# Kernel optimization log

Hardware: AMD Instinct MI355X
Metric: run time of the kernel (lower is better)

## Reference

```python
import jax, jax.numpy as jnp
import numpy as np
from jax import lax

H = 0.00048828125  # grid spacing h = 1/2048 (init kwarg)
B, G = 16, 2050    # batch, padded grid size; interior = G-2 = 2048


def _stencil(u, f_int, h2):
    # 4-neighbor Jacobi update on padded field u [B,1,G,G] -> [B,1,G-2,G-2]
    nbr = (u[..., :-2, 1:-1] + u[..., 2:, 1:-1] +
           u[..., 1:-1, :-2] + u[..., 1:-1, 2:])
    return (nbr + h2 * f_int) * 0.25


def setup_inputs() -> dict:
    key = jax.random.key(0)
    k1, k2 = jax.random.split(key)
    pre = jax.random.normal(k1, (B, 1, G, G), dtype=jnp.float32)
    f = jax.random.normal(k2, (B, 1, G, G), dtype=jnp.float32)
    return {"pre": pre, "f": f, "max_iter": 50}


def reference(pre, f, max_iter):
    h2 = jnp.asarray(H * H, dtype=pre.dtype)
    f_int = f[..., 1:-1, 1:-1]  # fixed interior source term

    w = _stencil(pre, f_int, h2)  # first step uses pre directly

    def body(w, _):
        # hard_encode: zero-pad border (gd = 0.0 default), then stencil step
        u = jnp.pad(w, ((0, 0), (0, 0), (1, 1), (1, 1)))
        return _stencil(u, f_int, h2), None

    w, _ = lax.scan(body, w, None, length=max_iter - 1)
    return w
```

## Files before the change

### kernel.cpp

```cpp
#include <hip/hip_runtime.h>


#define NDIM 2048
#define GDIM 2050
#define BATCH 16
#define H2 2.384185791015625e-07f

#define BSTRIDE 84
#define NSLOT 42

__device__ __forceinline__ float f4get(float4 v, int k) {
    return k == 0 ? v.x : k == 1 ? v.y : k == 2 ? v.z : v.w;
}

template<bool FIRST, bool EDGE>
__device__ __forceinline__ void run_block(const float* __restrict__ src,
                                          const float* __restrict__ fg,
                                          float* __restrict__ out, int iters,
                                          float* __restrict__ buf,
                                          float4* __restrict__ colL,
                                          float4* __restrict__ colR)
{
    const int tid = threadIdx.x;
    const int R0 = blockIdx.y * 64, C0 = blockIdx.x * 64;
    const int b = blockIdx.z;
    const float* sb = src + (size_t)b * (FIRST ? (size_t)GDIM * GDIM
                                               : (size_t)NDIM * NDIM);
    const float* fb = fg + (size_t)b * GDIM * GDIM;

    const bool active = tid < 400;
    const int cy = tid / 20, cx = tid - cy * 20;
    const int gy0 = R0 - 8 + 4 * cy, gx0 = C0 - 8 + 4 * cx;

    float cur[16], fv[16];
    unsigned mwb = 0;

    if (active) {
        if (!FIRST && !EDGE) {
            #pragma unroll
            for (int i = 0; i < 4; ++i) {
                float4 t = *(const float4*)&sb[(size_t)(gy0 + i) * NDIM + gx0];
                cur[i*4+0] = t.x; cur[i*4+1] = t.y;
                cur[i*4+2] = t.z; cur[i*4+3] = t.w;
            }
        } else {
            #pragma unroll
            for (int i = 0; i < 4; ++i) {
                #pragma unroll
                for (int j = 0; j < 4; ++j) {
                    int gy = gy0 + i, gx = gx0 + j;
                    float v = 0.0f;
                    if (FIRST) {
                        if (!EDGE || ((unsigned)(gy + 1) < (unsigned)GDIM &&
                                      (unsigned)(gx + 1) < (unsigned)GDIM))
                            v = sb[(size_t)(gy + 1) * GDIM + (gx + 1)];
                    } else {
                        if ((unsigned)gy < (unsigned)NDIM &&
                            (unsigned)gx < (unsigned)NDIM)
                            v = sb[(size_t)gy * NDIM + gx];
                    }
                    cur[i*4+j] = v;
                }
            }
        }
        #pragma unroll
        for (int i = 0; i < 4; ++i) {
            #pragma unroll
            for (int j = 0; j < 4; ++j) {
                int gy = gy0 + i, gx = gx0 + j;
                float vf = 0.0f;
                if (!EDGE) {
                    vf = fb[(size_t)(gy + 1) * GDIM + (gx + 1)];
                } else {
                    bool ok = (unsigned)gy < (unsigned)NDIM &&
                              (unsigned)gx < (unsigned)NDIM;
                    if (ok) vf = fb[(size_t)(gy + 1) * GDIM + (gx + 1)];
                    mwb |= (ok ? 1u : 0u) << (i*4+j);
                }
                fv[i*4+j] = vf;
            }
        }
        *(float4*)&buf[(2*cy+1)*BSTRIDE + 4*cx] =
            make_float4(cur[0], cur[1], cur[2], cur[3]);
        *(float4*)&buf[(2*cy+2)*BSTRIDE + 4*cx] =
            make_float4(cur[12], cur[13], cur[14], cur[15]);
        colL[cy*21+cx]     = make_float4(cur[0], cur[4], cur[8],  cur[12]);
        colR[cy*21+cx+1]   = make_float4(cur[3], cur[7], cur[11], cur[15]);
    } else if (tid < 480) {
        int role = (tid - 400) / 20;
        int k = tid - 400 - role * 20;
        float v[4];
        if (role < 2) {
            int gy = (role == 0) ? R0 - 9 : R0 + 72;
            int gxb = C0 - 8 + 4 * k;
            if (!FIRST && !EDGE) {
                float4 t = *(const float4*)&sb[(size_t)gy * NDIM + gxb];
                v[0] = t.x; v[1] = t.y; v[2] = t.z; v[3] = t.w;
            } else {
                #pragma unroll
                for (int j = 0; j < 4; ++j) {
                    int gx = gxb + j; float vv = 0.0f;
                    if (FIRST) {
                        if (!EDGE || ((unsigned)(gy + 1) < (unsigned)GDIM &&
                                      (unsigned)(gx + 1) < (unsigned)GDIM))
                            vv = sb[(size_t)(gy + 1) * GDIM + (gx + 1)];
                    } else {
                        if ((unsigned)gy < (unsigned)NDIM &&
                            (unsigned)gx < (unsigned)NDIM)
                            vv = sb[(size_t)gy * NDIM + gx];
                    }
                    v[j] = vv;
                }
            }
            int slot = (role == 0) ? 0 : (NSLOT - 1);
            *(float4*)&buf[slot * BSTRIDE + 4 * k] =
                make_float4(v[0], v[1], v[2], v[3]);
        } else {
            int gx = (role == 2) ? C0 - 9 : C0 + 72;
            int gyb = R0 - 8 + 4 * k;
            #pragma unroll
            for (int i = 0; i < 4; ++i) {
                int gy = gyb + i; float vv = 0.0f;
                if (FIRST) {
                    if (!EDGE || ((unsigned)(gy + 1) < (unsigned)GDIM &&
                                  (unsigned)(gx + 1) < (unsigned)GDIM))
                        vv = sb[(size_t)(gy + 1) * GDIM + (gx + 1)];
                } else {
                    if ((unsigned)gy < (unsigned)NDIM &&
                        (unsigned)gx < (unsigned)NDIM)
                        vv = sb[(size_t)gy * NDIM + gx];
                }
                v[i] = vv;
            }
            if (role == 2) colR[k*21 + 0]  = make_float4(v[0], v[1], v[2], v[3]);
            else           colL[k*21 + 20] = make_float4(v[0], v[1], v[2], v[3]);
        }
    }
    __syncthreads();

    for (int s = 0; s < iters; ++s) {
        float4 Nv, Sv, Wv, Ev;
        if (active) {
            Nv = *(const float4*)&buf[(2*cy)   * BSTRIDE + 4*cx];
            Sv = *(const float4*)&buf[(2*cy+3) * BSTRIDE + 4*cx];
            Wv = colR[cy*21+cx];
            Ev = colL[cy*21+cx+1];
        }
        __syncthreads();
        if (active) {
            float pn[4] = { Nv.x, Nv.y, Nv.z, Nv.w };
            #pragma unroll
            for (int i = 0; i < 4; ++i) {
                float t[4];
                #pragma unroll
                for (int j = 0; j < 4; ++j) {
                    float nn = pn[j];
                    float sv = (i == 3) ? f4get(Sv, j) : cur[(i+1)*4+j];
                    float wv = (j == 0) ? f4get(Wv, i) : cur[i*4+j-1];
                    float ev = (j == 3) ? f4get(Ev, i) : cur[i*4+j+1];
                    float val = (nn + sv + wv + ev + H2 * fv[i*4+j]) * 0.25f;
                    if (EDGE) val = ((mwb >> (i*4+j)) & 1u) ? val : 0.0f;
                    t[j] = val;
                }
                #pragma unroll
                for (int j = 0; j < 4; ++j) {
                    pn[j] = cur[i*4+j];
                    cur[i*4+j] = t[j];
                }
            }
            *(float4*)&buf[(2*cy+1)*BSTRIDE + 4*cx] =
                make_float4(cur[0], cur[1], cur[2], cur[3]);
            *(float4*)&buf[(2*cy+2)*BSTRIDE + 4*cx] =
                make_float4(cur[12], cur[13], cur[14], cur[15]);
            colL[cy*21+cx]   = make_float4(cur[0], cur[4], cur[8],  cur[12]);
            colR[cy*21+cx+1] = make_float4(cur[3], cur[7], cur[11], cur[15]);
        }
        __syncthreads();
    }

    if (active && cy >= 2 && cy < 18 && cx >= 2 && cx < 18) {
        float* ob = out + (size_t)b * NDIM * NDIM;
        const int oy0 = R0 + 4 * (cy - 2);
        const int ox0 = C0 + 4 * (cx - 2);
        #pragma unroll
        for (int i = 0; i < 4; ++i)
            *(float4*)&ob[(size_t)(oy0 + i) * NDIM + ox0] =
                make_float4(cur[i*4+0], cur[i*4+1], cur[i*4+2], cur[i*4+3]);
    }
}

template<bool FIRST>
__global__ __launch_bounds__(512)
void jacobi_fused(const float* __restrict__ src, const float* __restrict__ f,
                  float* __restrict__ out, int iters)
{
    __shared__ __align__(16) float buf[NSLOT * BSTRIDE];
    __shared__ float4 colL[20 * 21];
    __shared__ float4 colR[20 * 21];
    const bool edge = (blockIdx.x == 0) || (blockIdx.x == 31) ||
                      (blockIdx.y == 0) || (blockIdx.y == 31);
    if (edge) run_block<FIRST, true >(src, f, out, iters, buf, colL, colR);
    else      run_block<FIRST, false>(src, f, out, iters, buf, colL, colR);
}

extern "C" void kernel_launch(void* const* d_in, const int* in_sizes, int n_in,
                              void* d_out, int out_size, void* d_ws, size_t ws_size,
                              hipStream_t stream) {
    const float* pre = (const float*)d_in[0];
    const float* f   = (const float*)d_in[1];
    float* out = (float*)d_out;
    float* ws  = (float*)d_ws;

    dim3 block(512, 1, 1);
    dim3 grid(32, 32, BATCH);

    hipLaunchKernelGGL(jacobi_fused<true>,  grid, block, 0, stream, pre, f, ws,  9);
    hipLaunchKernelGGL(jacobi_fused<false>, grid, block, 0, stream, ws,  f, out, 9);
    hipLaunchKernelGGL(jacobi_fused<false>, grid, block, 0, stream, out, f, ws,  9);
    hipLaunchKernelGGL(jacobi_fused<false>, grid, block, 0, stream, ws,  f, out, 9);
    hipLaunchKernelGGL(jacobi_fused<false>, grid, block, 0, stream, out, f, ws,  9);
    hipLaunchKernelGGL(jacobi_fused<false>, grid, block, 0, stream, ws,  f, out, 5);
}
```

Measured before the change: 2.673 ms.

## Use 4x8 per-thread register tiles with 256-thread blocks in fused Jacobi

Each thread now holds an 8-row by 4-column tile in registers instead of 4x4, so a 256-thread block covers the same 80x80 halo tile with 200 compute threads. This halves the number of shared-memory halo exchanges per point and the number of participating threads per barrier, and it uses a launch bound of 256 threads with 4 blocks per CU. The shared-memory strides change and the row-halo loads lose their float4 fast path, since helper threads now loop over the 80 halo tasks. More registers per thread (32 cur plus 32 fv) could limit occupancy or cause spills.

Result: slower. 3.865 ms (+44.6%).

```diff
diff --git a/kernel.cpp b/kernel.cpp
--- a/kernel.cpp
+++ b/kernel.cpp
@@ -6,8 +6,9 @@
 #define BATCH 16
 #define H2 2.384185791015625e-07f
 
-#define BSTRIDE 84
-#define NSLOT 42
+#define BSTRIDE 88
+#define NSLOT 22
+#define CSTRIDE 28
 
 __device__ __forceinline__ float f4get(float4 v, int k) {
     return k == 0 ? v.x : k == 1 ? v.y : k == 2 ? v.z : v.w;
@@ -28,24 +29,24 @@
                                                : (size_t)NDIM * NDIM);
     const float* fb = fg + (size_t)b * GDIM * GDIM;
 
-    const bool active = tid < 400;
-    const int cy = tid / 20, cx = tid - cy * 20;
-    const int gy0 = R0 - 8 + 4 * cy, gx0 = C0 - 8 + 4 * cx;
-
-    float cur[16], fv[16];
+    const bool active = tid < 200;
+    const int chy = tid / 20, chx = tid - chy * 20;
+    const int gy0 = R0 - 8 + 8 * chy, gx0 = C0 - 8 + 4 * chx;
+
+    float cur[32], fv[32];
     unsigned mwb = 0;
 
     if (active) {
         if (!FIRST && !EDGE) {
             #pragma unroll
-            for (int i = 0; i < 4; ++i) {
+            for (int i = 0; i < 8; ++i) {
                 float4 t = *(const float4*)&sb[(size_t)(gy0 + i) * NDIM + gx0];
                 cur[i*4+0] = t.x; cur[i*4+1] = t.y;
                 cur[i*4+2] = t.z; cur[i*4+3] = t.w;
             }
         } else {
             #pragma unroll
-            for (int i = 0; i < 4; ++i) {
+            for (int i = 0; i < 8; ++i) {
                 #pragma unroll
                 for (int j = 0; j < 4; ++j) {
                     int gy = gy0 + i, gx = gx0 + j;
@@ -64,7 +65,7 @@
             }
         }
         #pragma unroll
-        for (int i = 0; i < 4; ++i) {
+        for (int i = 0; i < 8; ++i) {
             #pragma unroll
             for (int j = 0; j < 4; ++j) {
                 int gy = gy0 + i, gx = gx0 + j;
@@ -80,23 +81,22 @@
                 fv[i*4+j] = vf;
             }
         }
-        *(float4*)&buf[(2*cy+1)*BSTRIDE + 4*cx] =
+        *(float4*)&buf[(2*chy+1)*BSTRIDE + 4*chx] =
             make_float4(cur[0], cur[1], cur[2], cur[3]);
-        *(float4*)&buf[(2*cy+2)*BSTRIDE + 4*cx] =
-            make_float4(cur[12], cur[13], cur[14], cur[15]);
-        colL[cy*21+cx]     = make_float4(cur[0], cur[4], cur[8],  cur[12]);
-        colR[cy*21+cx+1]   = make_float4(cur[3], cur[7], cur[11], cur[15]);
-    } else if (tid < 480) {
-        int role = (tid - 400) / 20;
-        int k = tid - 400 - role * 20;
-        float v[4];
-        if (role < 2) {
-            int gy = (role == 0) ? R0 - 9 : R0 + 72;
-            int gxb = C0 - 8 + 4 * k;
-            if (!FIRST && !EDGE) {
-                float4 t = *(const float4*)&sb[(size_t)gy * NDIM + gxb];
-                v[0] = t.x; v[1] = t.y; v[2] = t.z; v[3] = t.w;
-            } else {
+        *(float4*)&buf[(2*chy+2)*BSTRIDE + 4*chx] =
+            make_float4(cur[28], cur[29], cur[30], cur[31]);
+        colL[(2*chy+0)*CSTRIDE + chx]   = make_float4(cur[0],  cur[4],  cur[8],  cur[12]);
+        colL[(2*chy+1)*CSTRIDE + chx]   = make_float4(cur[16], cur[20], cur[24], cur[28]);
+        colR[(2*chy+0)*CSTRIDE + chx+1] = make_float4(cur[3],  cur[7],  cur[11], cur[15]);
+        colR[(2*chy+1)*CSTRIDE + chx+1] = make_float4(cur[19], cur[23], cur[27], cur[31]);
+    } else {
+        for (int task = tid - 200; task < 80; task += 56) {
+            int kind = task / 20;
+            int k = task - kind * 20;
+            float v[4];
+            if (kind < 2) {
+                int gy = (kind == 0) ? R0 - 9 : R0 + 72;
+                int gxb = C0 - 8 + 4 * k;
                 #pragma unroll
                 for (int j = 0; j < 4; ++j) {
                     int gx = gxb + j; float vv = 0.0f;
@@ -111,53 +111,57 @@
                     }
                     v[j] = vv;
                 }
-            }
-            int slot = (role == 0) ? 0 : (NSLOT - 1);
-            *(float4*)&buf[slot * BSTRIDE + 4 * k] =
-                make_float4(v[0], v[1], v[2], v[3]);
-        } else {
-            int gx = (role == 2) ? C0 - 9 : C0 + 72;
-            int gyb = R0 - 8 + 4 * k;
-            #pragma unroll
-            for (int i = 0; i < 4; ++i) {
-                int gy = gyb + i; float vv = 0.0f;
-                if (FIRST) {
-                    if (!EDGE || ((unsigned)(gy + 1) < (unsigned)GDIM &&
-                                  (unsigned)(gx + 1) < (unsigned)GDIM))
-                        vv = sb[(size_t)(gy + 1) * GDIM + (gx + 1)];
-                } else {
-                    if ((unsigned)gy < (unsigned)NDIM &&
-                        (unsigned)gx < (unsigned)NDIM)
-                        vv = sb[(size_t)gy * NDIM + gx];
-                }
-                v[i] = vv;
-            }
-            if (role == 2) colR[k*21 + 0]  = make_float4(v[0], v[1], v[2], v[3]);
-            else           colL[k*21 + 20] = make_float4(v[0], v[1], v[2], v[3]);
+                int slot = (kind == 0) ? 0 : (NSLOT - 1);
+                *(float4*)&buf[slot * BSTRIDE + 4 * k] =
+                    make_float4(v[0], v[1], v[2], v[3]);
+            } else {
+                int gx = (kind == 2) ? C0 - 9 : C0 + 72;
+                int gyb = R0 - 8 + 4 * k;
+                #pragma unroll
+                for (int i = 0; i < 4; ++i) {
+                    int gy = gyb + i; float vv = 0.0f;
+                    if (FIRST) {
+                        if (!EDGE || ((unsigned)(gy + 1) < (unsigned)GDIM &&
+                                      (unsigned)(gx + 1) < (unsigned)GDIM))
+                            vv = sb[(size_t)(gy + 1) * GDIM + (gx + 1)];
+                    } else {
+                        if ((unsigned)gy < (unsigned)NDIM &&
+                            (unsigned)gx < (unsigned)NDIM)
+                            vv = sb[(size_t)gy * NDIM + gx];
+                    }
+                    v[i] = vv;
+                }
+                if (kind == 2) colR[k * CSTRIDE + 0]  = make_float4(v[0], v[1], v[2], v[3]);
+                else           colL[k * CSTRIDE + 20] = make_float4(v[0], v[1], v[2], v[3]);
+            }
         }
     }
     __syncthreads();
 
     for (int s = 0; s < iters; ++s) {
-        float4 Nv, Sv, Wv, Ev;
+        float4 Nv, Sv, Wv0, Wv1, Ev0, Ev1;
         if (active) {
-            Nv = *(const float4*)&buf[(2*cy)   * BSTRIDE + 4*cx];
-            Sv = *(const float4*)&buf[(2*cy+3) * BSTRIDE + 4*cx];
-            Wv = colR[cy*21+cx];
-            Ev = colL[cy*21+cx+1];
+            Nv  = *(const float4*)&buf[(2*chy)   * BSTRIDE + 4*chx];
+            Sv  = *(const float4*)&buf[(2*chy+3) * BSTRIDE + 4*chx];
+            Wv0 = colR[(2*chy+0)*CSTRIDE + chx];
+            Wv1 = colR[(2*chy+1)*CSTRIDE + chx];
+            Ev0 = colL[(2*chy+0)*CSTRIDE + chx+1];
+            Ev1 = colL[(2*chy+1)*CSTRIDE + chx+1];
         }
         __syncthreads();
         if (active) {
             float pn[4] = { Nv.x, Nv.y, Nv.z, Nv.w };
             #pragma unroll
-            for (int i = 0; i < 4; ++i) {
+            for (int i = 0; i < 8; ++i) {
                 float t[4];
                 #pragma unroll
                 for (int j = 0; j < 4; ++j) {
                     float nn = pn[j];
-                    float sv = (i == 3) ? f4get(Sv, j) : cur[(i+1)*4+j];
-                    float wv = (j == 0) ? f4get(Wv, i) : cur[i*4+j-1];
-                    float ev = (j == 3) ? f4get(Ev, i) : cur[i*4+j+1];
+                    float sv = (i == 7) ? f4get(Sv, j) : cur[(i+1)*4+j];
+                    float wv = (j == 0) ? f4get(i < 4 ? Wv0 : Wv1, i & 3)
+                                        : cur[i*4+j-1];
+                    float ev = (j == 3) ? f4get(i < 4 ? Ev0 : Ev1, i & 3)
+                                        : cur[i*4+j+1];
                     float val = (nn + sv + wv + ev + H2 * fv[i*4+j]) * 0.25f;
                     if (EDGE) val = ((mwb >> (i*4+j)) & 1u) ? val : 0.0f;
                     t[j] = val;
@@ -168,35 +172,37 @@
                     cur[i*4+j] = t[j];
                 }
             }
-            *(float4*)&buf[(2*cy+1)*BSTRIDE + 4*cx] =
+            *(float4*)&buf[(2*chy+1)*BSTRIDE + 4*chx] =
                 make_float4(cur[0], cur[1], cur[2], cur[3]);
-            *(float4*)&buf[(2*cy+2)*BSTRIDE + 4*cx] =
-                make_float4(cur[12], cur[13], cur[14], cur[15]);
-            colL[cy*21+cx]   = make_float4(cur[0], cur[4], cur[8],  cur[12]);
-            colR[cy*21+cx+1] = make_float4(cur[3], cur[7], cur[11], cur[15]);
+            *(float4*)&buf[(2*chy+2)*BSTRIDE + 4*chx] =
+                make_float4(cur[28], cur[29], cur[30], cur[31]);
+            colL[(2*chy+0)*CSTRIDE + chx]   = make_float4(cur[0],  cur[4],  cur[8],  cur[12]);
+            colL[(2*chy+1)*CSTRIDE + chx]   = make_float4(cur[16], cur[20], cur[24], cur[28]);
+            colR[(2*chy+0)*CSTRIDE + chx+1] = make_float4(cur[3],  cur[7],  cur[11], cur[15]);
+            colR[(2*chy+1)*CSTRIDE + chx+1] = make_float4(cur[19], cur[23], cur[27], cur[31]);
         }
         __syncthreads();
     }
 
-    if (active && cy >= 2 && cy < 18 && cx >= 2 && cx < 18) {
+    if (active && chy >= 1 && chy <= 8 && chx >= 2 && chx <= 17) {
         float* ob = out + (size_t)b * NDIM * NDIM;
-        const int oy0 = R0 + 4 * (cy - 2);
-        const int ox0 = C0 + 4 * (cx - 2);
+        const int oy0 = R0 + 8 * (chy - 1);
+        const int ox0 = C0 + 4 * (chx - 2);
         #pragma unroll
-        for (int i = 0; i < 4; ++i)
+        for (int i = 0; i < 8; ++i)
             *(float4*)&ob[(size_t)(oy0 + i) * NDIM + ox0] =
                 make_float4(cur[i*4+0], cur[i*4+1], cur[i*4+2], cur[i*4+3]);
     }
 }
 
 template<bool FIRST>
-__global__ __launch_bounds__(512)
+__global__ __launch_bounds__(256, 4)
 void jacobi_fused(const float* __restrict__ src, const float* __restrict__ f,
                   float* __restrict__ out, int iters)
 {
     __shared__ __align__(16) float buf[NSLOT * BSTRIDE];
-    __shared__ float4 colL[20 * 21];
-    __shared__ float4 colR[20 * 21];
+    __shared__ float4 colL[20 * CSTRIDE];
+    __shared__ float4 colR[20 * CSTRIDE];
     const bool edge = (blockIdx.x == 0) || (blockIdx.x == 31) ||
                       (blockIdx.y == 0) || (blockIdx.y == 31);
     if (edge) run_block<FIRST, true >(src, f, out, iters, buf, colL, colR);
@@ -211,7 +217,7 @@
     float* out = (float*)d_out;
     float* ws  = (float*)d_ws;
 
-    dim3 block(512, 1, 1);
+    dim3 block(256, 1, 1);
     dim3 grid(32, 32, BATCH);
 
     hipLaunchKernelGGL(jacobi_fused<true>,  grid, block, 0, stream, pre, f, ws,  9);
```
